# Optimization experiments

Hardware: AMD Instinct MI355X
Metric: run time of the kernel (lower is better)

Reference implementation:

```python
import jax, jax.numpy as jnp
import numpy as np

B, D, H = 64, 512, 512          # batch c, spatial dim D, feature dim H == channel
CIN = 4 * H                     # concat of 4 branches
HID = CIN // 4                  # reduction=4


def _gcn_norm_adj():
    # fixed 4-node fully-connected graph, GCNConv default: add self loops,
    # symmetric normalization D^{-1/2} (A+I) D^{-1/2}
    ei = np.array([[0, 1, 0, 2, 0, 3, 1, 2, 1, 3, 2, 3],
                   [1, 0, 2, 0, 3, 0, 2, 1, 3, 1, 3, 2]])
    A = np.zeros((4, 4), np.float32)
    A[ei[1], ei[0]] = 1.0               # message src -> dst
    A += np.eye(4, dtype=np.float32)    # self loops
    dinv = 1.0 / np.sqrt(A.sum(1))
    return jnp.asarray(dinv[:, None] * A * dinv[None, :])  # (4,4)


def setup_inputs() -> dict:
    key = jax.random.key(0)
    ks = jax.random.split(key, 32)

    def rn(k, shape, s=0.02):
        return jax.random.normal(k, shape, dtype=jnp.float32) * s

    inp = {}
    for i in range(4):
        inp[f"fea{i+1}"] = jax.random.normal(ks[i], (B, D, H), dtype=jnp.float32)
    inp["W_gcn"] = rn(ks[4], (H, H))
    inp["b_gcn"] = jnp.zeros((H,), jnp.float32)
    for i in range(4):
        inp[f"W1_{i+1}"] = rn(ks[5 + 4 * i], (CIN, HID))
        inp[f"b1_{i+1}"] = jnp.zeros((HID,), jnp.float32)
        inp[f"W2_{i+1}"] = rn(ks[6 + 4 * i], (HID, H))
        inp[f"b2_{i+1}"] = jnp.zeros((H,), jnp.float32)
    return inp


def reference(fea1, fea2, fea3, fea4, W_gcn, b_gcn,
              W1_1, b1_1, W2_1, b2_1,
              W1_2, b1_2, W2_2, b2_2,
              W1_3, b1_3, W2_3, b2_3,
              W1_4, b1_4, W2_4, b2_4):
    A = _gcn_norm_adj()                                   # (4,4)
    y = jnp.stack((fea1, fea2, fea3, fea4), axis=1)       # (B,4,D,H)
    # GCNConv batched over all samples: Ahat_norm @ (X W) + b
    xw = jnp.einsum('bndh,hk->bndk', y, W_gcn)            # (B,4,D,H)
    yg = jnp.einsum('mn,bndk->bmdk', A, xw) + b_gcn       # (B,4,D,H)
    z = jnp.concatenate([yg[:, 0], yg[:, 1], yg[:, 2], yg[:, 3]], axis=2)  # (B,D,4H)

    def gate(W1, b1, W2, b2, fea):
        h = jax.nn.relu(z @ W1 + b1)                      # (B,D,HID)
        g = jax.nn.sigmoid(h @ W2 + b2)                   # (B,D,H)
        return jax.nn.relu(g) * fea

    return (gate(W1_1, b1_1, W2_1, b2_1, fea1),
            gate(W1_2, b1_2, W2_2, b2_2, fea2),
            gate(W1_3, b1_3, W2_3, b2_3, fea3),
            gate(W1_4, b1_4, W2_4, b2_4, fea4))
```

## Files before the change

### kernel.cpp

```cpp
#include <hip/hip_runtime.h>
#include <math.h>

#define MM 32768
#define KK 512
#define NN 512
#define BM 128
#define BN 128
#define BK 32

typedef float  f32x4  __attribute__((ext_vector_type(4)));
typedef __bf16 bf16x8 __attribute__((ext_vector_type(8)));
typedef unsigned short u16x8 __attribute__((ext_vector_type(8)));
typedef unsigned short u16x4 __attribute__((ext_vector_type(4)));

__device__ __forceinline__ unsigned short f2bf(float f) {
    union { float f; unsigned int u; } v; v.f = f;
    unsigned int r = v.u + 0x7fffu + ((v.u >> 16) & 1u);
    return (unsigned short)(r >> 16);
}

__device__ __forceinline__ float bf2f(unsigned short h) {
    union { unsigned int u; float f; } v; v.u = ((unsigned int)h) << 16;
    return v.f;
}

__device__ __forceinline__ void gl_lds16(const void* g, void* l) {
    __builtin_amdgcn_global_load_lds((const __attribute__((address_space(1))) void*)g,
                                     (__attribute__((address_space(3))) void*)l,
                                     16, 0, 0);
}

__global__ __launch_bounds__(256)
void fsum_cast(const float* __restrict__ f1, const float* __restrict__ f2,
               const float* __restrict__ f3, const float* __restrict__ f4,
               unsigned short* __restrict__ out)
{
    const long i = ((long)blockIdx.x * 256 + threadIdx.x) * 8;
    f32x4 s0 = *(const f32x4*)(f1 + i);
    f32x4 s1 = *(const f32x4*)(f1 + i + 4);
    s0 += *(const f32x4*)(f2 + i);  s1 += *(const f32x4*)(f2 + i + 4);
    s0 += *(const f32x4*)(f3 + i);  s1 += *(const f32x4*)(f3 + i + 4);
    s0 += *(const f32x4*)(f4 + i);  s1 += *(const f32x4*)(f4 + i + 4);
    u16x8 o;
    o[0] = f2bf(s0[0]); o[1] = f2bf(s0[1]); o[2] = f2bf(s0[2]); o[3] = f2bf(s0[3]);
    o[4] = f2bf(s1[0]); o[5] = f2bf(s1[1]); o[6] = f2bf(s1[2]); o[7] = f2bf(s1[3]);
    *(u16x8*)(out + i) = o;
}

struct WArgs {
    const float* src[9];
    unsigned short* dst[9];
};

__global__ __launch_bounds__(256)
void wprep(WArgs a)
{
    __shared__ float t[32][33];
    const int z  = blockIdx.z;
    const float* __restrict__ src = a.src[z];
    unsigned short* __restrict__ dst = a.dst[z];
    const int k0 = blockIdx.x * 32;
    const int n0 = blockIdx.y * 32;
    const int tx = threadIdx.x;
    if (z == 0) {
        for (int kk = threadIdx.y; kk < 32; kk += 8) {
            float v = src[(long)(k0 + kk) * 512 + n0 + tx];
            dst[(long)(k0 + kk) * 512 + n0 + tx] = f2bf(0.25f * v);
        }
        return;
    }
    for (int kk = threadIdx.y; kk < 32; kk += 8) {
        float v = src[(long)(k0 + kk) * 512 + n0 + tx];
        if (z >= 1 && z <= 4) {
            v += src[(long)(512  + k0 + kk) * 512 + n0 + tx];
            v += src[(long)(1024 + k0 + kk) * 512 + n0 + tx];
            v += src[(long)(1536 + k0 + kk) * 512 + n0 + tx];
        }
        t[kk][tx] = v;
    }
    __syncthreads();
    for (int nn = threadIdx.y; nn < 32; nn += 8) {
        dst[(long)(n0 + nn) * 512 + k0 + tx] = f2bf(t[tx][nn]);
    }
}

struct BArgs {
    const unsigned short* w1t[4];
    const float* b1[4];
    float* out[4];
};

__global__ __launch_bounds__(256)
void bprep(const float* __restrict__ bg, BArgs a)
{
    __shared__ float bgs[512];
    const int z = blockIdx.x;
    const int tid = threadIdx.x;
    bgs[tid]       = bg[tid];
    bgs[tid + 256] = bg[tid + 256];
    __syncthreads();
    const unsigned short* __restrict__ w = a.w1t[z];
    for (int n = tid; n < 512; n += 256) {
        float acc = 0.0f;
        const unsigned short* row = w + (long)n * 512;
        #pragma unroll 4
        for (int t = 0; t < 512; t += 8) {
            u16x8 wv = *(const u16x8*)(row + t);
            #pragma unroll
            for (int jj = 0; jj < 8; ++jj) acc += bgs[t + jj] * bf2f(wv[jj]);
        }
        a.out[z][n] = acc + a.b1[z][n];
    }
}

struct GArgs {
    const unsigned short* A[4];
    const unsigned short* Bt[4];
    const float* bias[4];
    const float* fea[4];
    void* out[4];
};

__device__ __forceinline__ void stage4(const unsigned short* gb, unsigned short* lb, int r) {
    #pragma unroll
    for (int c = 0; c < 4; ++c)
        gl_lds16(gb + (long)(c * 16 + r) * KK, lb + c * 16 * BK);
}

template<int MODE>
__global__ __launch_bounds__(256)
void gemm_ep(GArgs a)
{
    __shared__ unsigned short As[2][BM * BK];
    __shared__ unsigned short Bs[2][BN * BK];

    const int z = blockIdx.z;
    const unsigned short* __restrict__ A  = a.A[z];
    const unsigned short* __restrict__ Bt = a.Bt[z];
    const float* __restrict__ bias = a.bias[z];
    const float* __restrict__ fea  = a.fea[z];
    void* __restrict__ out = a.out[z];

    const int tid  = threadIdx.x;
    const int lane = tid & 63;
    const int wave = tid >> 6;
    const int m0 = blockIdx.x * BM;
    const int n0 = blockIdx.y * BN;

    const bool isA = (wave < 2);
    const int rowbase = (wave & 1) * 64;
    const unsigned short* gsrc = isA ? A : Bt;
    const int r  = lane >> 2;
    const int cb = lane & 3;
    const long grow0 = (isA ? (long)m0 : (long)n0) + rowbase;
    const unsigned short* gbase0 = gsrc + grow0 * KK + cb * 8;
    unsigned short* lb0 = (isA ? As[0] : Bs[0]) + rowbase * BK;
    unsigned short* lb1 = (isA ? As[1] : Bs[1]) + rowbase * BK;

    const int frow = lane & 15;
    const int fk   = (lane >> 4) * 8;
    const int wrow = wave >> 1;
    const int wcol = wave & 1;

    f32x4 acc[4][4] = {};

    stage4(gbase0, lb0, r);
    __syncthreads();

    #pragma unroll 2
    for (int ks = 0; ks < KK / BK; ++ks) {
        const bool odd = (ks & 1);
        if (ks + 1 < KK / BK)
            stage4(gbase0 + (ks + 1) * BK, odd ? lb0 : lb1, r);

        const unsigned short* Asc = odd ? As[1] : As[0];
        const unsigned short* Bsc = odd ? Bs[1] : Bs[0];
        bf16x8 afr[4], bfr[4];
        #pragma unroll
        for (int i = 0; i < 4; ++i)
            afr[i] = *(const bf16x8*)(Asc + (wrow * 64 + i * 16 + frow) * BK + fk);
        #pragma unroll
        for (int j = 0; j < 4; ++j)
            bfr[j] = *(const bf16x8*)(Bsc + (wcol * 64 + j * 16 + frow) * BK + fk);

        #pragma unroll
        for (int i = 0; i < 4; ++i)
            #pragma unroll
            for (int j = 0; j < 4; ++j)
                acc[i][j] = __builtin_amdgcn_mfma_f32_16x16x32_bf16(
                    bfr[j], afr[i], acc[i][j], 0, 0, 0);

        __syncthreads();
    }

    const int mr  = lane & 15;
    const int cq4 = (lane >> 4) * 4;
    #pragma unroll
    for (int j = 0; j < 4; ++j) {
        const int col = n0 + wcol * 64 + j * 16 + cq4;
        f32x4 bv;
        if (MODE == 3) { bv[0] = bv[1] = bv[2] = bv[3] = 0.0f; }
        else           { bv = *(const f32x4*)(bias + col); }
        #pragma unroll
        for (int i = 0; i < 4; ++i) {
            const long row = m0 + wrow * 64 + i * 16 + mr;
            f32x4 v = acc[i][j] + bv;
            if (MODE == 1) {
                u16x4 o;
                o[0] = f2bf(fmaxf(v[0], 0.0f)); o[1] = f2bf(fmaxf(v[1], 0.0f));
                o[2] = f2bf(fmaxf(v[2], 0.0f)); o[3] = f2bf(fmaxf(v[3], 0.0f));
                *(u16x4*)((unsigned short*)out + row * NN + col) = o;
            } else if (MODE == 3) {
                u16x4 o;
                o[0] = f2bf(v[0]); o[1] = f2bf(v[1]);
                o[2] = f2bf(v[2]); o[3] = f2bf(v[3]);
                *(u16x4*)((unsigned short*)out + row * NN + col) = o;
            } else {
                f32x4 fv = *(const f32x4*)(fea + row * NN + col);
                f32x4 o;
                #pragma unroll
                for (int q = 0; q < 4; ++q) {
                    float e = __expf(-v[q]);
                    o[q] = __fdividef(fv[q], 1.0f + e);
                }
                *(f32x4*)((float*)out + row * NN + col) = o;
            }
        }
    }
}

extern "C" void kernel_launch(void* const* d_in, const int* in_sizes, int n_in,
                              void* d_out, int out_size, void* d_ws, size_t ws_size,
                              hipStream_t stream)
{
    (void)in_sizes; (void)n_in; (void)out_size; (void)ws_size;

    const float* fea[4] = {(const float*)d_in[0], (const float*)d_in[1],
                           (const float*)d_in[2], (const float*)d_in[3]};
    const float* W_gcn = (const float*)d_in[4];
    const float* b_gcn = (const float*)d_in[5];
    const float *W1[4], *b1[4], *W2[4], *b2[4];
    for (int i = 0; i < 4; ++i) {
        W1[i] = (const float*)d_in[6 + 4 * i];
        b1[i] = (const float*)d_in[7 + 4 * i];
        W2[i] = (const float*)d_in[8 + 4 * i];
        b2[i] = (const float*)d_in[9 + 4 * i];
    }

    const size_t MB = 1024 * 1024;
    char* ws = (char*)d_ws;
    unsigned short* fsum_h = (unsigned short*)ws;
    unsigned short* wbuf   = (unsigned short*)(ws + 32 * MB);
    unsigned short* Wgb = wbuf;
    unsigned short *W1T[4], *W2T[4], *WcT[4], *hbuf[4];
    for (int i = 0; i < 4; ++i) {
        W1T[i] = wbuf + (size_t)(1 + i) * 262144;
        W2T[i] = wbuf + (size_t)(5 + i) * 262144;
        WcT[i] = (unsigned short*)(ws + 40 * MB) + (size_t)i * 262144;
        hbuf[i] = (unsigned short*)(ws + 48 * MB + (size_t)i * 32 * MB);
    }
    float* bcomb = (float*)(ws + 44 * MB);

    fsum_cast<<<8192, 256, 0, stream>>>(fea[0], fea[1], fea[2], fea[3], fsum_h);

    WArgs wa;
    wa.src[0] = W_gcn; wa.dst[0] = Wgb;
    for (int i = 0; i < 4; ++i) { wa.src[1 + i] = W1[i]; wa.dst[1 + i] = W1T[i]; }
    for (int i = 0; i < 4; ++i) { wa.src[5 + i] = W2[i]; wa.dst[5 + i] = W2T[i]; }
    wprep<<<dim3(16, 16, 9), dim3(32, 8), 0, stream>>>(wa);

    BArgs ba;
    for (int i = 0; i < 4; ++i) { ba.w1t[i] = W1T[i]; ba.b1[i] = b1[i]; ba.out[i] = bcomb + (size_t)i * 512; }
    bprep<<<4, 256, 0, stream>>>(b_gcn, ba);

    GArgs g3;
    for (int i = 0; i < 4; ++i) {
        g3.A[i] = W1T[i]; g3.Bt[i] = Wgb; g3.bias[i] = nullptr;
        g3.fea[i] = nullptr; g3.out[i] = WcT[i];
    }
    gemm_ep<3><<<dim3(4, 4, 4), 256, 0, stream>>>(g3);

    GArgs g1;
    for (int i = 0; i < 4; ++i) {
        g1.A[i] = fsum_h; g1.Bt[i] = WcT[i]; g1.bias[i] = bcomb + (size_t)i * 512;
        g1.fea[i] = nullptr; g1.out[i] = hbuf[i];
    }
    gemm_ep<1><<<dim3(MM / BM, NN / BN, 4), 256, 0, stream>>>(g1);

    float* outp = (float*)d_out;
    GArgs g2;
    for (int i = 0; i < 4; ++i) {
        g2.A[i] = hbuf[i]; g2.Bt[i] = W2T[i]; g2.bias[i] = b2[i];
        g2.fea[i] = fea[i]; g2.out[i] = outp + (size_t)i * MM * NN;
    }
    gemm_ep<2><<<dim3(MM / BM, NN / BN, 4), 256, 0, stream>>>(g2);
}
```

Measured before the change: 838.6 us.

## Triple-buffer GEMM LDS staging with explicit vmcnt waits and XOR swizzle

Moves the GEMM main loop from two LDS buffers to three, with two tiles prefetched ahead. Each step uses manual s_waitcnt vmcnt counts and raw barriers in place of __syncthreads. It also XOR-swizzles the 16-byte chunk index on both the global-to-LDS copy and the fragment reads to cut LDS bank conflicts. The aim is to hide global load latency and speed up LDS reads. The cost is more LDS per block, which may lower occupancy, and correctness now depends on the hand-tuned wait counts.

```diff
diff --git a/kernel.cpp b/kernel.cpp
--- a/kernel.cpp
+++ b/kernel.cpp
@@ -7,6 +7,7 @@
 #define BM 128
 #define BN 128
 #define BK 32
+#define NT (KK / BK)
 
 typedef float  f32x4  __attribute__((ext_vector_type(4)));
 typedef __bf16 bf16x8 __attribute__((ext_vector_type(8)));
@@ -131,8 +132,8 @@
 __global__ __launch_bounds__(256)
 void gemm_ep(GArgs a)
 {
-    __shared__ unsigned short As[2][BM * BK];
-    __shared__ unsigned short Bs[2][BN * BK];
+    __shared__ __attribute__((aligned(16))) unsigned short As[3][BM * BK];
+    __shared__ __attribute__((aligned(16))) unsigned short Bs[3][BN * BK];
 
     const int z = blockIdx.z;
     const unsigned short* __restrict__ A  = a.A[z];
@@ -150,31 +151,37 @@
     const bool isA = (wave < 2);
     const int rowbase = (wave & 1) * 64;
     const unsigned short* gsrc = isA ? A : Bt;
-    const int r  = lane >> 2;
-    const int cb = lane & 3;
+    const int r   = lane >> 2;
+    const int cb  = lane & 3;
+    const int cbs = cb ^ ((r >> 1) & 3);
     const long grow0 = (isA ? (long)m0 : (long)n0) + rowbase;
-    const unsigned short* gbase0 = gsrc + grow0 * KK + cb * 8;
-    unsigned short* lb0 = (isA ? As[0] : Bs[0]) + rowbase * BK;
-    unsigned short* lb1 = (isA ? As[1] : Bs[1]) + rowbase * BK;
+    const unsigned short* gbase0 = gsrc + grow0 * KK + cbs * 8;
+    unsigned short* lb[3] = {
+        (isA ? As[0] : Bs[0]) + rowbase * BK,
+        (isA ? As[1] : Bs[1]) + rowbase * BK,
+        (isA ? As[2] : Bs[2]) + rowbase * BK };
 
     const int frow = lane & 15;
-    const int fk   = (lane >> 4) * 8;
+    const int fk   = ((lane >> 4) ^ ((frow >> 1) & 3)) * 8;
     const int wrow = wave >> 1;
     const int wcol = wave & 1;
 
     f32x4 acc[4][4] = {};
 
-    stage4(gbase0, lb0, r);
-    __syncthreads();
-
-    #pragma unroll 2
-    for (int ks = 0; ks < KK / BK; ++ks) {
-        const bool odd = (ks & 1);
-        if (ks + 1 < KK / BK)
-            stage4(gbase0 + (ks + 1) * BK, odd ? lb0 : lb1, r);
-
-        const unsigned short* Asc = odd ? As[1] : As[0];
-        const unsigned short* Bsc = odd ? Bs[1] : Bs[0];
+    stage4(gbase0 + 0 * BK, lb[0], r);
+    stage4(gbase0 + 1 * BK, lb[1], r);
+    stage4(gbase0 + 2 * BK, lb[2], r);
+
+    #pragma unroll
+    for (int ks = 0; ks < NT; ++ks) {
+        if      (ks < NT - 2) asm volatile("s_waitcnt vmcnt(8)" ::: "memory");
+        else if (ks == NT - 2) asm volatile("s_waitcnt vmcnt(4)" ::: "memory");
+        else                   asm volatile("s_waitcnt vmcnt(0)" ::: "memory");
+        __builtin_amdgcn_s_barrier();
+        asm volatile("" ::: "memory");
+
+        const unsigned short* Asc = As[ks % 3];
+        const unsigned short* Bsc = Bs[ks % 3];
         bf16x8 afr[4], bfr[4];
         #pragma unroll
         for (int i = 0; i < 4; ++i)
@@ -190,7 +197,11 @@
                 acc[i][j] = __builtin_amdgcn_mfma_f32_16x16x32_bf16(
                     bfr[j], afr[i], acc[i][j], 0, 0, 0);
 
-        __syncthreads();
+        asm volatile("" ::: "memory");
+        __builtin_amdgcn_s_barrier();
+        asm volatile("" ::: "memory");
+        if (ks + 3 < NT)
+            stage4(gbase0 + (ks + 3) * BK, lb[ks % 3], r);
     }
 
     const int mr  = lane & 15;
```

After: 828.9 us. No clear change (-1.2%).
